# Optimization experiments

Hardware: AMD Instinct MI355X
Metric: run time of the kernel (lower is better)

Reference implementation:

```python
import jax, jax.numpy as jnp
import numpy as np

# Module constants (from init_kwargs)
K_BUDGET = 16      # selector budget K
R_REFRAC = 1       # refractory separation r
LAM = 0.5          # selector regularization lambda
MAX_PROXY = 64     # max_proxy_points (K_eff cap)


def setup_inputs() -> dict:
    key = jax.random.key(0)
    ks = jax.random.split(key, 8)
    B, T, D = 32, 4096, 128
    H, K_LIFT, D_MODEL = 256, 64, 1024
    g = lambda i, shape, s=0.05: jax.random.normal(ks[i], shape, jnp.float32) * s
    return {
        "x": jax.random.normal(ks[0], (B, T, D), jnp.float32),
        "W1": g(1, (D, H)),
        "b1": jnp.zeros((H,), jnp.float32),
        "w_e": g(2, (H,)),
        "w_s": g(3, (H,)),
        "W_lift": g(4, (D + 3, K_LIFT)),
        "b_lift": jnp.zeros((K_LIFT,), jnp.float32),
        "W_proj": g(5, (K_LIFT, D_MODEL)),
        "b_proj": jnp.zeros((D_MODEL,), jnp.float32),
        "log_temperature": jnp.zeros((), jnp.float32),
    }


def _soft_selector(saliency, log_temperature):
    """SoftSelectorProxy.forward: sigmoid relaxation of budget+refractory QP."""
    T = saliency.shape[1]
    temp = jnp.clip(jnp.exp(log_temperature), 0.1, 10.0)
    logits = (saliency / (2.0 * LAM) - 0.5) / temp
    y = jax.nn.sigmoid(logits)
    y = y.at[:, 0].set(0.0)
    budget = jnp.clip(y.sum(axis=1, keepdims=True), 1e-6)
    y = y * jnp.minimum(K_BUDGET / budget, 1.0)
    for d in range(1, min(R_REFRAC + 1, T)):  # r=1 -> single unrolled step
        pair_sum = y + jnp.roll(y, -d, axis=1)
        y = y * jnp.minimum(2.0 / (1.0 + pair_sum), 1.0)
    y = y.at[:, 0].set(0.0)
    return y


def reference(x, W1, b1, w_e, w_s, W_lift, b_lift, W_proj, b_proj, log_temperature):
    B, T, D = x.shape
    # 1. CausalEventModel: per-step MLP -> event scores + saliency  [B,T]
    h = jnp.tanh(jnp.einsum("btd,dh->bth", x, W1) + b1)
    event_scores = h @ w_e                       # [B,T] (unused downstream)
    saliency = jax.nn.softplus(h @ w_s)          # [B,T], nonnegative saliency
    # 2. Relaxed selector proxy -> continuous anchor weights y*  [B,T]
    y_star = _soft_selector(saliency, log_temperature)
    # 3. Dense anchor vectors: x augmented with 3 topology features (anchor_dim = D+3)
    tpos = jnp.broadcast_to(jnp.arange(T, dtype=x.dtype) / T, (B, T))
    cums = jnp.cumsum(saliency, axis=1)
    dense = jnp.concatenate(
        [x, saliency[..., None], tpos[..., None], cums[..., None]], axis=-1
    )  # [B,T,D+3]
    # 4. NormalizedLift: linear lift to k dims, L2-normalized cloud  [B,T,k]
    lifted = jnp.einsum("bta,ak->btk", dense, W_lift) + b_lift
    lifted = lifted / jnp.clip(
        jnp.linalg.norm(lifted, axis=-1, keepdims=True), 1e-6
    )
    # 5. Top-K anchor selection + gather + projection  [B,K_eff,d_model]
    K_eff = min(T, MAX_PROXY)
    _, top_idx = jax.lax.top_k(y_star, K_eff)                 # [B,K_eff]
    cloud = jnp.take_along_axis(lifted, top_idx[..., None], axis=1)  # [B,K_eff,k]
    tokens = jnp.einsum("bnk,kd->bnd", cloud, W_proj) + b_proj
    return tokens, y_star
```

## Files before the change

kernel.cpp:

```cpp
#include <hip/hip_runtime.h>
#include <math.h>

#define TT 4096
#define BB 32
#define DD 128
#define HH 256
#define KL 64
#define DM 1024
#define KEFF 64
#define KBUDGET 16.0f
#define LAM_ 0.5f

__global__ __launch_bounds__(256, 2) void k_sal(const float* __restrict__ x,
    const float* __restrict__ W1, const float* __restrict__ b1,
    const float* __restrict__ w_s, float* __restrict__ sal_out)
{
  __shared__ float xs[64][DD + 4];
  __shared__ float w1s[DD][64];

  const int tid = threadIdx.x;
  const long rowbase = (long)blockIdx.x * 64;

  {
    const float4* xg = (const float4*)(x + rowbase * DD);
    #pragma unroll
    for (int it = 0; it < 8; ++it) {
      int i = tid + it * 256;
      int r = i >> 5, c4 = i & 31;
      float4 v = xg[i];
      *(float4*)&xs[r][c4 * 4] = v;
    }
  }

  const int lane = tid & 63;
  const int wave = tid >> 6;
  const int hq = lane & 15;
  const int rq = lane >> 4;
  const int rb = wave * 16 + rq * 4;

  float s_acc[4] = {0.f, 0.f, 0.f, 0.f};

  for (int c = 0; c < HH / 64; ++c) {
    __syncthreads();
    #pragma unroll
    for (int it = 0; it < 8; ++it) {
      int i = tid + it * 256;
      int h4 = i & 15, d = i >> 4;
      float4 v = *(const float4*)&W1[d * HH + c * 64 + h4 * 4];
      *(float4*)&w1s[d][h4 * 4] = v;
    }
    __syncthreads();

    float acc[4][4];
    #pragma unroll
    for (int i = 0; i < 4; ++i)
      #pragma unroll
      for (int j = 0; j < 4; ++j) acc[i][j] = 0.f;

    #pragma unroll 2
    for (int d4 = 0; d4 < DD / 4; ++d4) {
      float4 xv0 = *(const float4*)&xs[rb + 0][d4 * 4];
      float4 xv1 = *(const float4*)&xs[rb + 1][d4 * 4];
      float4 xv2 = *(const float4*)&xs[rb + 2][d4 * 4];
      float4 xv3 = *(const float4*)&xs[rb + 3][d4 * 4];
      float4 wv0 = *(const float4*)&w1s[d4 * 4 + 0][hq * 4];
      float4 wv1 = *(const float4*)&w1s[d4 * 4 + 1][hq * 4];
      float4 wv2 = *(const float4*)&w1s[d4 * 4 + 2][hq * 4];
      float4 wv3 = *(const float4*)&w1s[d4 * 4 + 3][hq * 4];
#define ROWFMA(I, XV)                                  \
      acc[I][0] = fmaf(XV.x, wv0.x, acc[I][0]);        \
      acc[I][1] = fmaf(XV.x, wv0.y, acc[I][1]);        \
      acc[I][2] = fmaf(XV.x, wv0.z, acc[I][2]);        \
      acc[I][3] = fmaf(XV.x, wv0.w, acc[I][3]);        \
      acc[I][0] = fmaf(XV.y, wv1.x, acc[I][0]);        \
      acc[I][1] = fmaf(XV.y, wv1.y, acc[I][1]);        \
      acc[I][2] = fmaf(XV.y, wv1.z, acc[I][2]);        \
      acc[I][3] = fmaf(XV.y, wv1.w, acc[I][3]);        \
      acc[I][0] = fmaf(XV.z, wv2.x, acc[I][0]);        \
      acc[I][1] = fmaf(XV.z, wv2.y, acc[I][1]);        \
      acc[I][2] = fmaf(XV.z, wv2.z, acc[I][2]);        \
      acc[I][3] = fmaf(XV.z, wv2.w, acc[I][3]);        \
      acc[I][0] = fmaf(XV.w, wv3.x, acc[I][0]);        \
      acc[I][1] = fmaf(XV.w, wv3.y, acc[I][1]);        \
      acc[I][2] = fmaf(XV.w, wv3.z, acc[I][2]);        \
      acc[I][3] = fmaf(XV.w, wv3.w, acc[I][3]);
      ROWFMA(0, xv0)
      ROWFMA(1, xv1)
      ROWFMA(2, xv2)
      ROWFMA(3, xv3)
#undef ROWFMA
    }

    const int h0 = c * 64 + hq * 4;
    #pragma unroll
    for (int j = 0; j < 4; ++j) {
      float bj = b1[h0 + j];
      float wsj = w_s[h0 + j];
      #pragma unroll
      for (int i = 0; i < 4; ++i) {
        float t = tanhf(acc[i][j] + bj);
        s_acc[i] = fmaf(t, wsj, s_acc[i]);
      }
    }
  }

  #pragma unroll
  for (int m = 1; m < 16; m <<= 1) {
    #pragma unroll
    for (int i = 0; i < 4; ++i) s_acc[i] += __shfl_xor(s_acc[i], m, 64);
  }
  if (hq == 0) {
    #pragma unroll
    for (int i = 0; i < 4; ++i) {
      float z = s_acc[i];
      float sp = fmaxf(z, 0.f) + log1pf(expf(-fabsf(z)));
      sal_out[rowbase + rb + i] = sp;
    }
  }
}

__global__ __launch_bounds__(256) void k_sel(const float* __restrict__ logt,
    float* __restrict__ ysr, int* __restrict__ topidx,
    float* __restrict__ topsal, float* __restrict__ topcums)
{
  __shared__ float sal[TT];
  __shared__ float ya[TT];
  __shared__ float yb[TT];
  __shared__ float redf[8];
  __shared__ int   redi[8];

  const int tid = threadIdx.x;
  const int lane = tid & 63;
  const int wave = tid >> 6;
  const int b = blockIdx.x;
  float* row = ysr + (long)b * TT;

  for (int i = tid; i < TT; i += 256) sal[i] = row[i];
  __syncthreads();

  float temp = expf(logt[0]);
  temp = fminf(fmaxf(temp, 0.1f), 10.f);
  const float inv2lam = 1.0f / (2.0f * LAM_);

  for (int i = tid; i < TT; i += 256) {
    float z = (sal[i] * inv2lam - 0.5f) / temp;
    float s;
    if (z >= 0.f) { float e = expf(-z); s = 1.f / (1.f + e); }
    else          { float e = expf(z);  s = e / (1.f + e); }
    ya[i] = (i == 0) ? 0.f : s;
  }
  __syncthreads();

  float loc = 0.f;
  for (int i = tid; i < TT; i += 256) loc += ya[i];
  #pragma unroll
  for (int m = 1; m < 64; m <<= 1) loc += __shfl_xor(loc, m, 64);
  if (lane == 0) redf[wave] = loc;
  __syncthreads();
  float budget = redf[0] + redf[1] + redf[2] + redf[3];
  float scale = fminf(KBUDGET / fmaxf(budget, 1e-6f), 1.f);

  for (int i = tid; i < TT; i += 256) {
    float yi = ya[i] * scale;
    float yj = ya[(i + 1) & (TT - 1)] * scale;
    float m = fminf(2.f / (1.f + (yi + yj)), 1.f);
    yb[i] = (i == 0) ? 0.f : yi * m;
  }
  __syncthreads();

  for (int i = tid; i < TT; i += 256) row[i] = yb[i];

  const int base = tid * 16;
  float run = 0.f;
  #pragma unroll
  for (int j = 0; j < 16; ++j) { run += sal[base + j]; ya[base + j] = run; }
  float v = run;
  #pragma unroll
  for (int m = 1; m < 64; m <<= 1) {
    float u = __shfl_up(v, (unsigned)m, 64);
    if (lane >= m) v += u;
  }
  float lexcl = v - run;
  if (lane == 63) redf[4 + wave] = v;
  __syncthreads();
  float woff = 0.f;
  for (int w = 0; w < wave; ++w) woff += redf[4 + w];
  float off = woff + lexcl;
  #pragma unroll
  for (int j = 0; j < 16; ++j) ya[base + j] += off;
  __syncthreads();

  float lv[16];
  #pragma unroll
  for (int j = 0; j < 16; ++j) lv[j] = yb[base + j];
  unsigned rm = 0;
  float bv = -1.f; int bi = 1 << 30;
  #pragma unroll
  for (int j = 0; j < 16; ++j)
    if (!((rm >> j) & 1u) && lv[j] > bv) { bv = lv[j]; bi = base + j; }

  for (int it = 0; it < KEFF; ++it) {
    float cv = bv; int ci = bi;
    #pragma unroll
    for (int m = 1; m < 64; m <<= 1) {
      float ov = __shfl_xor(cv, m, 64);
      int   oi = __shfl_xor(ci, m, 64);
      if (ov > cv || (ov == cv && oi < ci)) { cv = ov; ci = oi; }
    }
    if (lane == 0) { redf[wave] = cv; redi[wave] = ci; }
    __syncthreads();
    float wv_ = redf[0]; int wi_ = redi[0];
    #pragma unroll
    for (int w = 1; w < 4; ++w)
      if (redf[w] > wv_ || (redf[w] == wv_ && redi[w] < wi_)) { wv_ = redf[w]; wi_ = redi[w]; }
    if (tid == 0) {
      topidx[b * KEFF + it]  = wi_;
      topsal[b * KEFF + it]  = sal[wi_];
      topcums[b * KEFF + it] = ya[wi_];
    }
    if (wi_ >= base && wi_ < base + 16) {
      rm |= 1u << (wi_ - base);
      bv = -1.f; bi = 1 << 30;
      #pragma unroll
      for (int j = 0; j < 16; ++j)
        if (!((rm >> j) & 1u) && lv[j] > bv) { bv = lv[j]; bi = base + j; }
    }
    __syncthreads();
  }
}

__global__ __launch_bounds__(256) void k_tok(const float* __restrict__ x,
    const float* __restrict__ W_lift, const float* __restrict__ b_lift,
    const float* __restrict__ W_proj, const float* __restrict__ b_proj,
    const int* __restrict__ topidx, const float* __restrict__ topsal,
    const float* __restrict__ topcums, float* __restrict__ tokens)
{
  __shared__ float cloud[8][KL];
  const int tid = threadIdx.x;
  const int k = tid & 63;
  const int g = tid >> 6;
  const int b = blockIdx.x >> 3;
  const int nb = (blockIdx.x & 7) * 8;

  #pragma unroll
  for (int a = 0; a < 2; ++a) {
    int n = nb + g + a * 4;
    int t = topidx[b * KEFF + n];
    const float* xr = x + ((long)b * TT + t) * DD;
    float acc = 0.f;
    #pragma unroll 8
    for (int d4 = 0; d4 < DD / 4; ++d4) {
      float4 xv = *(const float4*)&xr[d4 * 4];
      acc = fmaf(xv.x, W_lift[(d4 * 4 + 0) * KL + k], acc);
      acc = fmaf(xv.y, W_lift[(d4 * 4 + 1) * KL + k], acc);
      acc = fmaf(xv.z, W_lift[(d4 * 4 + 2) * KL + k], acc);
      acc = fmaf(xv.w, W_lift[(d4 * 4 + 3) * KL + k], acc);
    }
    float s  = topsal[b * KEFF + n];
    float tp = (float)t / (float)TT;
    float cm = topcums[b * KEFF + n];
    acc = fmaf(s,  W_lift[128 * KL + k], acc);
    acc = fmaf(tp, W_lift[129 * KL + k], acc);
    acc = fmaf(cm, W_lift[130 * KL + k], acc);
    acc += b_lift[k];
    float ss = acc * acc;
    #pragma unroll
    for (int m = 1; m < 64; m <<= 1) ss += __shfl_xor(ss, m, 64);
    float denom = fmaxf(sqrtf(ss), 1e-6f);
    cloud[g + a * 4][k] = acc / denom;
  }
  __syncthreads();

  #pragma unroll
  for (int q = 0; q < 4; ++q) {
    int dcol = tid + q * 256;
    float accp[8];
    #pragma unroll
    for (int n = 0; n < 8; ++n) accp[n] = 0.f;
    for (int kk = 0; kk < KL; ++kk) {
      float w = W_proj[kk * DM + dcol];
      #pragma unroll
      for (int n = 0; n < 8; ++n) accp[n] = fmaf(cloud[n][kk], w, accp[n]);
    }
    float bp = b_proj[dcol];
    #pragma unroll
    for (int n = 0; n < 8; ++n)
      tokens[((long)b * KEFF + nb + n) * DM + dcol] = accp[n] + bp;
  }
}

extern "C" void kernel_launch(void* const* d_in, const int* in_sizes, int n_in,
                              void* d_out, int out_size, void* d_ws, size_t ws_size,
                              hipStream_t stream) {
  const float* x      = (const float*)d_in[0];
  const float* W1     = (const float*)d_in[1];
  const float* b1     = (const float*)d_in[2];
  const float* w_s    = (const float*)d_in[4];
  const float* W_lift = (const float*)d_in[5];
  const float* b_lift = (const float*)d_in[6];
  const float* W_proj = (const float*)d_in[7];
  const float* b_proj = (const float*)d_in[8];
  const float* logt   = (const float*)d_in[9];

  float* tokens = (float*)d_out;
  float* ysr    = tokens + (size_t)BB * KEFF * DM;
  int*   topidx  = (int*)d_ws;
  float* topsal  = (float*)((char*)d_ws + 8192);
  float* topcums = (float*)((char*)d_ws + 16384);

  k_sal<<<(BB * TT) / 64, 256, 0, stream>>>(x, W1, b1, w_s, ysr);
  k_sel<<<BB, 256, 0, stream>>>(logt, ysr, topidx, topsal, topcums);
  k_tok<<<BB * 8, 256, 0, stream>>>(x, W_lift, b_lift, W_proj, b_proj,
                                    topidx, topsal, topcums, tokens);
}
```

Before: 266.7 us.

## Restructure saliency GEMM tiling, use fast tanh, and merge per-wave top-k lists

The saliency kernel drops the shared-memory W1 tiles. Each thread now computes an 8x8 tile over a 64-row by 256-hidden block, reading W1 straight from global/L1, with a cross-wave shared reduction and occupancy hint raised to 3. tanhf is replaced by an exp2/rcp approximation. The selection kernel has each wave find its own local top-64 independently with no block barriers per iteration, then one thread merges the four sorted lists. This removes 128 barriers per block at the cost of a serial merge and slightly different tanh accuracy.

```diff
diff --git a/kernel.cpp b/kernel.cpp
--- a/kernel.cpp
+++ b/kernel.cpp
@@ -11,111 +11,126 @@
 #define KBUDGET 16.0f
 #define LAM_ 0.5f
 
-__global__ __launch_bounds__(256, 2) void k_sal(const float* __restrict__ x,
+__device__ __forceinline__ float fast_tanh(float x) {
+#if __has_builtin(__builtin_amdgcn_exp2f)
+  float e = __builtin_amdgcn_exp2f(x * 2.885390081777927f);
+#else
+  float e = __expf(2.0f * x);
+#endif
+  float r = __builtin_amdgcn_rcpf(e + 1.0f);
+  return fmaf(-2.0f, r, 1.0f);
+}
+
+__global__ __launch_bounds__(256, 3) void k_sal(const float* __restrict__ x,
     const float* __restrict__ W1, const float* __restrict__ b1,
     const float* __restrict__ w_s, float* __restrict__ sal_out)
 {
-  __shared__ float xs[64][DD + 4];
-  __shared__ float w1s[DD][64];
-
-  const int tid = threadIdx.x;
-  const long rowbase = (long)blockIdx.x * 64;
-
-  {
-    const float4* xg = (const float4*)(x + rowbase * DD);
-    #pragma unroll
-    for (int it = 0; it < 8; ++it) {
-      int i = tid + it * 256;
-      int r = i >> 5, c4 = i & 31;
-      float4 v = xg[i];
-      *(float4*)&xs[r][c4 * 4] = v;
-    }
-  }
-
+  __shared__ float xs[64][132];
+  __shared__ float redsm[4][64];
+
+  const int tid  = threadIdx.x;
   const int lane = tid & 63;
   const int wave = tid >> 6;
-  const int hq = lane & 15;
-  const int rq = lane >> 4;
-  const int rb = wave * 16 + rq * 4;
-
-  float s_acc[4] = {0.f, 0.f, 0.f, 0.f};
-
-  for (int c = 0; c < HH / 64; ++c) {
-    __syncthreads();
-    #pragma unroll
-    for (int it = 0; it < 8; ++it) {
-      int i = tid + it * 256;
-      int h4 = i & 15, d = i >> 4;
-      float4 v = *(const float4*)&W1[d * HH + c * 64 + h4 * 4];
-      *(float4*)&w1s[d][h4 * 4] = v;
-    }
-    __syncthreads();
-
-    float acc[4][4];
-    #pragma unroll
-    for (int i = 0; i < 4; ++i)
-      #pragma unroll
-      for (int j = 0; j < 4; ++j) acc[i][j] = 0.f;
-
-    #pragma unroll 2
-    for (int d4 = 0; d4 < DD / 4; ++d4) {
-      float4 xv0 = *(const float4*)&xs[rb + 0][d4 * 4];
-      float4 xv1 = *(const float4*)&xs[rb + 1][d4 * 4];
-      float4 xv2 = *(const float4*)&xs[rb + 2][d4 * 4];
-      float4 xv3 = *(const float4*)&xs[rb + 3][d4 * 4];
-      float4 wv0 = *(const float4*)&w1s[d4 * 4 + 0][hq * 4];
-      float4 wv1 = *(const float4*)&w1s[d4 * 4 + 1][hq * 4];
-      float4 wv2 = *(const float4*)&w1s[d4 * 4 + 2][hq * 4];
-      float4 wv3 = *(const float4*)&w1s[d4 * 4 + 3][hq * 4];
-#define ROWFMA(I, XV)                                  \
-      acc[I][0] = fmaf(XV.x, wv0.x, acc[I][0]);        \
-      acc[I][1] = fmaf(XV.x, wv0.y, acc[I][1]);        \
-      acc[I][2] = fmaf(XV.x, wv0.z, acc[I][2]);        \
-      acc[I][3] = fmaf(XV.x, wv0.w, acc[I][3]);        \
-      acc[I][0] = fmaf(XV.y, wv1.x, acc[I][0]);        \
-      acc[I][1] = fmaf(XV.y, wv1.y, acc[I][1]);        \
-      acc[I][2] = fmaf(XV.y, wv1.z, acc[I][2]);        \
-      acc[I][3] = fmaf(XV.y, wv1.w, acc[I][3]);        \
-      acc[I][0] = fmaf(XV.z, wv2.x, acc[I][0]);        \
-      acc[I][1] = fmaf(XV.z, wv2.y, acc[I][1]);        \
-      acc[I][2] = fmaf(XV.z, wv2.z, acc[I][2]);        \
-      acc[I][3] = fmaf(XV.z, wv2.w, acc[I][3]);        \
-      acc[I][0] = fmaf(XV.w, wv3.x, acc[I][0]);        \
-      acc[I][1] = fmaf(XV.w, wv3.y, acc[I][1]);        \
-      acc[I][2] = fmaf(XV.w, wv3.z, acc[I][2]);        \
-      acc[I][3] = fmaf(XV.w, wv3.w, acc[I][3]);
-      ROWFMA(0, xv0)
-      ROWFMA(1, xv1)
-      ROWFMA(2, xv2)
-      ROWFMA(3, xv3)
-#undef ROWFMA
-    }
-
-    const int h0 = c * 64 + hq * 4;
-    #pragma unroll
-    for (int j = 0; j < 4; ++j) {
-      float bj = b1[h0 + j];
-      float wsj = w_s[h0 + j];
-      #pragma unroll
-      for (int i = 0; i < 4; ++i) {
-        float t = tanhf(acc[i][j] + bj);
-        s_acc[i] = fmaf(t, wsj, s_acc[i]);
-      }
-    }
-  }
-
-  #pragma unroll
-  for (int m = 1; m < 16; m <<= 1) {
-    #pragma unroll
-    for (int i = 0; i < 4; ++i) s_acc[i] += __shfl_xor(s_acc[i], m, 64);
+  const int rq = lane & 7;
+  const int hq = lane >> 3;
+  const int h0 = wave * 64 + hq * 8;
+  const long rowbase = (long)blockIdx.x * 64;
+
+  #pragma unroll
+  for (int p = 0; p < 8; ++p) {
+    int i = tid + p * 256;
+    int r = i >> 5, c4 = i & 31;
+    float4 v = *(const float4*)&x[(rowbase + r) * DD + c4 * 4];
+    *(float4*)&xs[r][c4 * 4] = v;
+  }
+  __syncthreads();
+
+  float acc[8][8];
+  #pragma unroll
+  for (int i = 0; i < 8; ++i)
+    #pragma unroll
+    for (int j = 0; j < 8; ++j) acc[i][j] = 0.f;
+
+  const float* __restrict__ Wb = W1 + h0;
+
+#define FMAROW(I, XD, WA, WB)                      \
+  acc[I][0] = fmaf(XD, WA.x, acc[I][0]);           \
+  acc[I][1] = fmaf(XD, WA.y, acc[I][1]);           \
+  acc[I][2] = fmaf(XD, WA.z, acc[I][2]);           \
+  acc[I][3] = fmaf(XD, WA.w, acc[I][3]);           \
+  acc[I][4] = fmaf(XD, WB.x, acc[I][4]);           \
+  acc[I][5] = fmaf(XD, WB.y, acc[I][5]);           \
+  acc[I][6] = fmaf(XD, WB.z, acc[I][6]);           \
+  acc[I][7] = fmaf(XD, WB.w, acc[I][7]);
+#define FMAD(C, WA, WB)                            \
+  FMAROW(0, xv0.C, WA, WB)                         \
+  FMAROW(1, xv1.C, WA, WB)                         \
+  FMAROW(2, xv2.C, WA, WB)                         \
+  FMAROW(3, xv3.C, WA, WB)                         \
+  FMAROW(4, xv4.C, WA, WB)                         \
+  FMAROW(5, xv5.C, WA, WB)                         \
+  FMAROW(6, xv6.C, WA, WB)                         \
+  FMAROW(7, xv7.C, WA, WB)
+
+  #pragma unroll 2
+  for (int d4 = 0; d4 < DD / 4; ++d4) {
+    float4 xv0 = *(const float4*)&xs[rq +  0][d4 * 4];
+    float4 xv1 = *(const float4*)&xs[rq +  8][d4 * 4];
+    float4 xv2 = *(const float4*)&xs[rq + 16][d4 * 4];
+    float4 xv3 = *(const float4*)&xs[rq + 24][d4 * 4];
+    float4 xv4 = *(const float4*)&xs[rq + 32][d4 * 4];
+    float4 xv5 = *(const float4*)&xs[rq + 40][d4 * 4];
+    float4 xv6 = *(const float4*)&xs[rq + 48][d4 * 4];
+    float4 xv7 = *(const float4*)&xs[rq + 56][d4 * 4];
+    const float* wp = Wb + (d4 * 4) * HH;
+    float4 wa0 = *(const float4*)&wp[0];
+    float4 wb0 = *(const float4*)&wp[4];
+    float4 wa1 = *(const float4*)&wp[HH];
+    float4 wb1 = *(const float4*)&wp[HH + 4];
+    float4 wa2 = *(const float4*)&wp[2 * HH];
+    float4 wb2 = *(const float4*)&wp[2 * HH + 4];
+    float4 wa3 = *(const float4*)&wp[3 * HH];
+    float4 wb3 = *(const float4*)&wp[3 * HH + 4];
+    FMAD(x, wa0, wb0)
+    FMAD(y, wa1, wb1)
+    FMAD(z, wa2, wb2)
+    FMAD(w, wa3, wb3)
+  }
+#undef FMAD
+#undef FMAROW
+
+  float4 ba  = *(const float4*)&b1[h0];
+  float4 bb  = *(const float4*)&b1[h0 + 4];
+  float4 wsa = *(const float4*)&w_s[h0];
+  float4 wsb = *(const float4*)&w_s[h0 + 4];
+  float s_acc[8];
+  #pragma unroll
+  for (int i = 0; i < 8; ++i) {
+    float s = 0.f;
+    s = fmaf(fast_tanh(acc[i][0] + ba.x), wsa.x, s);
+    s = fmaf(fast_tanh(acc[i][1] + ba.y), wsa.y, s);
+    s = fmaf(fast_tanh(acc[i][2] + ba.z), wsa.z, s);
+    s = fmaf(fast_tanh(acc[i][3] + ba.w), wsa.w, s);
+    s = fmaf(fast_tanh(acc[i][4] + bb.x), wsb.x, s);
+    s = fmaf(fast_tanh(acc[i][5] + bb.y), wsb.y, s);
+    s = fmaf(fast_tanh(acc[i][6] + bb.z), wsb.z, s);
+    s = fmaf(fast_tanh(acc[i][7] + bb.w), wsb.w, s);
+    s_acc[i] = s;
+  }
+  #pragma unroll
+  for (int m = 8; m < 64; m <<= 1) {
+    #pragma unroll
+    for (int i = 0; i < 8; ++i) s_acc[i] += __shfl_xor(s_acc[i], m, 64);
   }
   if (hq == 0) {
     #pragma unroll
-    for (int i = 0; i < 4; ++i) {
-      float z = s_acc[i];
-      float sp = fmaxf(z, 0.f) + log1pf(expf(-fabsf(z)));
-      sal_out[rowbase + rb + i] = sp;
-    }
+    for (int i = 0; i < 8; ++i) redsm[wave][rq + 8 * i] = s_acc[i];
+  }
+  __syncthreads();
+  if (tid < 64) {
+    float z = redsm[0][tid] + redsm[1][tid] + redsm[2][tid] + redsm[3][tid];
+    float sp = fmaxf(z, 0.f) + log1pf(expf(-fabsf(z)));
+    sal_out[rowbase + tid] = sp;
   }
 }
 
@@ -127,7 +142,8 @@
   __shared__ float ya[TT];
   __shared__ float yb[TT];
   __shared__ float redf[8];
-  __shared__ int   redi[8];
+  __shared__ float wl_val[4][KEFF];
+  __shared__ int   wl_idx[4][KEFF];
 
   const int tid = threadIdx.x;
   const int lane = tid & 63;
@@ -190,14 +206,15 @@
   for (int j = 0; j < 16; ++j) ya[base + j] += off;
   __syncthreads();
 
+  const int qb = wave * 1024 + lane * 16;
   float lv[16];
   #pragma unroll
-  for (int j = 0; j < 16; ++j) lv[j] = yb[base + j];
+  for (int j = 0; j < 16; ++j) lv[j] = yb[qb + j];
   unsigned rm = 0;
   float bv = -1.f; int bi = 1 << 30;
   #pragma unroll
   for (int j = 0; j < 16; ++j)
-    if (!((rm >> j) & 1u) && lv[j] > bv) { bv = lv[j]; bi = base + j; }
+    if (lv[j] > bv) { bv = lv[j]; bi = qb + j; }
 
   for (int it = 0; it < KEFF; ++it) {
     float cv = bv; int ci = bi;
@@ -207,25 +224,34 @@
       int   oi = __shfl_xor(ci, m, 64);
       if (ov > cv || (ov == cv && oi < ci)) { cv = ov; ci = oi; }
     }
-    if (lane == 0) { redf[wave] = cv; redi[wave] = ci; }
-    __syncthreads();
-    float wv_ = redf[0]; int wi_ = redi[0];
-    #pragma unroll
-    for (int w = 1; w < 4; ++w)
-      if (redf[w] > wv_ || (redf[w] == wv_ && redi[w] < wi_)) { wv_ = redf[w]; wi_ = redi[w]; }
-    if (tid == 0) {
-      topidx[b * KEFF + it]  = wi_;
-      topsal[b * KEFF + it]  = sal[wi_];
-      topcums[b * KEFF + it] = ya[wi_];
-    }
-    if (wi_ >= base && wi_ < base + 16) {
-      rm |= 1u << (wi_ - base);
+    if (lane == 0) { wl_val[wave][it] = cv; wl_idx[wave][it] = ci; }
+    if (ci >= qb && ci < qb + 16) {
+      rm |= 1u << (ci - qb);
       bv = -1.f; bi = 1 << 30;
       #pragma unroll
       for (int j = 0; j < 16; ++j)
-        if (!((rm >> j) & 1u) && lv[j] > bv) { bv = lv[j]; bi = base + j; }
-    }
-    __syncthreads();
+        if (!((rm >> j) & 1u) && lv[j] > bv) { bv = lv[j]; bi = qb + j; }
+    }
+  }
+  __syncthreads();
+
+  if (tid == 0) {
+    int p0 = 0, p1 = 0, p2 = 0, p3 = 0;
+    float v0 = wl_val[0][0], v1 = wl_val[1][0], v2 = wl_val[2][0], v3 = wl_val[3][0];
+    int   i0 = wl_idx[0][0], i1 = wl_idx[1][0], i2 = wl_idx[2][0], i3 = wl_idx[3][0];
+    for (int it = 0; it < KEFF; ++it) {
+      float va = v0; int ia = i0; int sa = 0;
+      if (v1 > va || (v1 == va && i1 < ia)) { va = v1; ia = i1; sa = 1; }
+      if (v2 > va || (v2 == va && i2 < ia)) { va = v2; ia = i2; sa = 2; }
+      if (v3 > va || (v3 == va && i3 < ia)) { va = v3; ia = i3; sa = 3; }
+      topidx[b * KEFF + it]  = ia;
+      topsal[b * KEFF + it]  = sal[ia];
+      topcums[b * KEFF + it] = ya[ia];
+      if      (sa == 0) { ++p0; v0 = (p0 < KEFF) ? wl_val[0][p0] : -1.f; i0 = (p0 < KEFF) ? wl_idx[0][p0] : (1 << 30); }
+      else if (sa == 1) { ++p1; v1 = (p1 < KEFF) ? wl_val[1][p1] : -1.f; i1 = (p1 < KEFF) ? wl_idx[1][p1] : (1 << 30); }
+      else if (sa == 2) { ++p2; v2 = (p2 < KEFF) ? wl_val[2][p2] : -1.f; i2 = (p2 < KEFF) ? wl_idx[2][p2] : (1 << 30); }
+      else              { ++p3; v3 = (p3 < KEFF) ? wl_val[3][p3] : -1.f; i3 = (p3 < KEFF) ? wl_idx[3][p3] : (1 << 30); }
+    }
   }
 }
 
```

Result: faster. 235.3 us (-11.8%).
